# Kernel tuning notes

Measured on AMD Instinct MI355X. Metric: run time of the kernel, lower is better.

## Reference

```python
import jax, jax.numpy as jnp
import numpy as np

N_DOC, N_WORD, N_ENT, N_POS = 10000, 20000, 10000, 60
D, D_POS_IN, D_WEMB = 128, 60, 300
E11, E22, E33, E01, E02, E03 = 320000, 160000, 3600, 300000, 100000, 150000
EPS = 1e-9


def spmm(rows, cols, vals, x, n_out):
    """Sparse (n_out x n_in) adjacency @ x via gather + weighted segment-sum."""
    return jax.ops.segment_sum(vals[:, None] * x[cols], rows, num_segments=n_out)


def gcn(rows, cols, vals, x, n_out, W=None, b=None):
    """GCN layer: adj @ (x W + b) with ReLU; identity=True in torch == W is None."""
    h = x if W is None else x @ W + b
    return jax.nn.relu(spmm(rows, cols, vals, h, n_out))


def setup_inputs():
    key = jax.random.key(0)
    ks = iter(jax.random.split(key, 64))
    randn = lambda s: jax.random.normal(next(ks), s, jnp.float32)
    rand = lambda s: jax.random.uniform(next(ks), s, dtype=jnp.float32)
    ridx = lambda s, hi: jax.random.randint(next(ks), s, 0, hi, jnp.int32)
    return {
        "f1": randn((N_WORD, D)),
        "f2": randn((N_ENT, D)),
        "f3": randn((N_POS, D_POS_IN)),
        "word_emb": randn((N_ENT, D_WEMB)),
        "a11_rows": ridx((E11,), N_WORD), "a11_cols": ridx((E11,), N_WORD), "a11_vals": rand((E11,)),
        "a22_rows": ridx((E22,), N_ENT), "a22_cols": ridx((E22,), N_ENT), "a22_vals": rand((E22,)),
        "a33_rows": ridx((E33,), N_POS), "a33_cols": ridx((E33,), N_POS), "a33_vals": rand((E33,)),
        "a01_rows": ridx((E01,), N_DOC), "a01_cols": ridx((E01,), N_WORD), "a01_vals": rand((E01,)),
        "a02_rows": ridx((E02,), N_DOC), "a02_cols": ridx((E02,), N_ENT), "a02_vals": rand((E02,)),
        "a03_rows": ridx((E03,), N_DOC), "a03_cols": ridx((E03,), N_POS), "a03_vals": rand((E03,)),
        "W3": randn((D_POS_IN, D)) * 0.1, "b3": jnp.zeros((D,), jnp.float32),
        "W1_2": randn((D, D)) * 0.1, "b1_2": jnp.zeros((D,), jnp.float32),
        "W2_2": randn((D, D)) * 0.1, "b2_2": jnp.zeros((D,), jnp.float32),
        "W3_2": randn((D, D)) * 0.1, "b3_2": jnp.zeros((D,), jnp.float32),
    }


def reference(f1, f2, f3, word_emb,
              a11_rows, a11_cols, a11_vals, a22_rows, a22_cols, a22_vals,
              a33_rows, a33_cols, a33_vals, a01_rows, a01_cols, a01_vals,
              a02_rows, a02_cols, a02_vals, a03_rows, a03_cols, a03_vals,
              W3, b3, W1_2, b1_2, W2_2, b2_2, W3_2, b3_2):
    # eval mode: F.dropout(training=False) is a no-op
    # type 1 (words): GCN(identity=True) -> GCN_2
    h1 = gcn(a11_rows, a11_cols, a11_vals, f1, N_WORD)
    h1 = gcn(a11_rows, a11_cols, a11_vals, h1, N_WORD, W1_2, b1_2)
    # type 2 (entities, concat_word_emb=True): GCN(identity=True) -> GCN_2 -> concat word_emb
    h2 = gcn(a22_rows, a22_cols, a22_vals, f2, N_ENT)
    h2 = gcn(a22_rows, a22_cols, a22_vals, h2, N_ENT, W2_2, b2_2)
    h2 = jnp.concatenate([h2, word_emb], axis=-1)  # [N_ENT, D + D_WEMB]
    # type 3 (POS): full GCN -> GCN_2
    h3 = gcn(a33_rows, a33_cols, a33_vals, f3, N_POS, W3, b3)
    h3 = gcn(a33_rows, a33_cols, a33_vals, h3, N_POS, W3_2, b3_2)
    # cross-type aggregation onto documents + L2 normalization
    outs = []
    for rows, cols, vals, h in ((a01_rows, a01_cols, a01_vals, h1),
                                (a02_rows, a02_cols, a02_vals, h2),
                                (a03_rows, a03_cols, a03_vals, h3)):
        agg = spmm(rows, cols, vals, h, N_DOC)  # [N_DOC, d]
        outs.append(agg / (jnp.linalg.norm(agg, axis=-1, keepdims=True) + EPS))
    return tuple(outs)
```

## Files before the change

kernel.cpp:

```cpp
#include <hip/hip_runtime.h>
#include <hip/hip_bf16.h>

typedef __hip_bfloat16 bf16;

#define N_DOC   10000
#define N_WORD  20000
#define N_ENT   10000
#define N_POS   60
#define DD      128
#define D_WEMB  300
#define E11     320000
#define E22     160000
#define E33     3600
#define E01     300000
#define E02     100000
#define E03     150000

#define ROFF11  0
#define ROFF22  20000
#define ROFF33  30000
#define ROFF01  30060
#define ROFF02  40060
#define ROFF03  50060
#define NROWS   60060
#define EOFF11  0
#define EOFF22  320000
#define EOFF33  480000
#define EOFF01  483600
#define EOFF02  783600
#define EOFF03  883600
#define NEDGES  1033600

#define BSHIFT  9
#define NBUCK   118
#define BCAP    18432
#define P1_TILE 4096
#define P1_EPT  8
#define NB1K    253
#define NCONV   120
#define NPOSB1  15

#define HFO_STAGE   0
#define HFO_PAIRS   4349952
#define HFO_G       5383552
#define HFO_BCUR    5443616
#define HFO_F1B     5443744
#define HFO_F2B     6723744
#define HFO_WEMBB   7363744
#define HFO_S0B     8863744
#define HFO_S1B     10143744
#define HFO_E0B     11423744
#define HFO_E1B     12063744
#define HFO_P3A     12703744
#define HFO_P3B     12711424
#define HFO_END     12719104

__device__ __forceinline__ float loadf(const void* p, size_t i, int isb) {
    return isb ? __bfloat162float(((const bf16*)p)[i])
               : ((const float*)p)[i];
}
__device__ __forceinline__ float b2f(unsigned u16) {
    union { unsigned v; float f; } x; x.v = u16 << 16; return x.f;
}
__device__ __forceinline__ unsigned f2b(float f) {
    bf16 h = __float2bfloat16(f);
    union { bf16 h; unsigned short u; } x; x.h = h; return (unsigned)x.u;
}
__device__ __forceinline__ void storef(void* p, size_t i, int asb, float v) {
    if (asb) ((unsigned short*)p)[i] = (unsigned short)f2b(v);
    else     ((float*)p)[i] = v;
}
__device__ __forceinline__ unsigned pack_pair(int col, float v) {
    return (f2b(v) << 16) | (unsigned)col;
}

__device__ __forceinline__ void edge_decode(
        int i,
        const int* __restrict__ r11, const int* __restrict__ c11, const void* __restrict__ v11,
        const int* __restrict__ r22, const int* __restrict__ c22, const void* __restrict__ v22,
        const int* __restrict__ r33, const int* __restrict__ c33, const void* __restrict__ v33,
        const int* __restrict__ r01, const int* __restrict__ c01, const void* __restrict__ v01,
        const int* __restrict__ r02, const int* __restrict__ c02, const void* __restrict__ v02,
        const int* __restrict__ r03, const int* __restrict__ c03, const void* __restrict__ v03,
        int isb, int& slot, int& col, float& val) {
    if      (i < EOFF22) { int k = i;          slot = ROFF11 + r11[k]; col = c11[k]; val = loadf(v11, k, isb); }
    else if (i < EOFF33) { int k = i - EOFF22; slot = ROFF22 + r22[k]; col = c22[k]; val = loadf(v22, k, isb); }
    else if (i < EOFF01) { int k = i - EOFF33; slot = ROFF33 + r33[k]; col = c33[k]; val = loadf(v33, k, isb); }
    else if (i < EOFF02) { int k = i - EOFF01; slot = ROFF01 + r01[k]; col = c01[k]; val = loadf(v01, k, isb); }
    else if (i < EOFF03) { int k = i - EOFF02; slot = ROFF02 + r02[k]; col = c02[k]; val = loadf(v02, k, isb); }
    else                 { int k = i - EOFF03; slot = ROFF03 + r03[k]; col = c03[k]; val = loadf(v03, k, isb); }
}

__global__ void detect_kernel(const unsigned* __restrict__ probe, int* __restrict__ flag,
                              int* __restrict__ bcur) {
    __shared__ int cnt;
    if (threadIdx.x == 0) cnt = 0;
    __syncthreads();
    int insane = 0;
    for (int i = threadIdx.x; i < 1024; i += 256) {
        float x = __uint_as_float(probe[i]);
        float a = fabsf(x);
        if (!(a > 1e-10f && a < 1e10f)) insane++;
    }
    atomicAdd(&cnt, insane);
    if (bcur && threadIdx.x < NBUCK) bcur[threadIdx.x] = threadIdx.x * BCAP;
    __syncthreads();
    if (threadIdx.x == 0) *flag = (cnt > 512) ? 1 : 0;
}

__device__ __forceinline__ void conv_seg(const void* __restrict__ src,
                                         unsigned* __restrict__ dst,
                                         int npairs, int isb, int tid, int stride) {
    if (isb) {
        const unsigned* s = (const unsigned*)src;
        for (int i = tid; i < npairs; i += stride) dst[i] = s[i];
    } else {
        const float2* s = (const float2*)src;
        for (int i = tid; i < npairs; i += stride) {
            float2 x = s[i];
            dst[i] = f2b(x.x) | (f2b(x.y) << 16);
        }
    }
}

template<bool RELU, int K>
__device__ __forceinline__ void rowpar_body256(
        const void* __restrict__ X, int xisb,
        const void* __restrict__ W, const void* __restrict__ b,
        void* __restrict__ out, int oisb, int isb,
        int row, int tid, float* xr ) {
    int half = tid >> 7;
    int j = tid & 127;
    float* xrh = xr + half * K;
    if (j < K) {
        float x = loadf(X, (size_t)row * K + j, xisb);
        if (RELU) x = fmaxf(x, 0.f);
        xrh[j] = x;
    }
    __syncthreads();
    float acc = loadf(b, j, isb);
    #pragma unroll 8
    for (int k = 0; k < K; ++k)
        acc = fmaf(xrh[k], loadf(W, (size_t)k * 128 + j, isb), acc);
    storef(out, (size_t)row * 128 + j, oisb, acc);
}

template<bool RELU, int K>
__device__ __forceinline__ void rowpar_body512(
        const void* __restrict__ X, int xisb,
        const void* __restrict__ W, const void* __restrict__ b,
        void* __restrict__ out, int oisb, int isb,
        int row0, int tid, float* xr ) {
    int q = tid >> 7;
    int j = tid & 127;
    int row = row0 + q;
    float* xrh = xr + q * K;
// ... 136 lines not shown
        wsum2[t] = v;
    }
    __syncthreads();
    int myrp = ((w > 0) ? wsum2[w - 1] : 0) + s - x;
    rp[t] = myrp;
    cu[t] = 0;
    int slot = (b << BSHIFT) + t;
    if (slot < NROWS) G[slot] = bb + myrp;
    __syncthreads();
    for (int i = t; i < cnt; i += 512) {
        uint2 r = st[i];
        int sl = (r.x >> 16) & 511;
        int p = atomicAdd(&cu[sl], 1);
        pairs[bb + rp[sl] + p] = (r.y << 16) | (r.x & 0xffffu);
    }
}

__global__ void hist2_kernel(const int* __restrict__ rowsA, int nEA,
                             const int* __restrict__ rowsB, int nEB,
                             int nA, int* __restrict__ cnt) {
    int i = blockIdx.x * blockDim.x + threadIdx.x;
    if (i < nEA) atomicAdd(cnt + rowsA[i], 1);
    else if (i < nEA + nEB) atomicAdd(cnt + nA + rowsB[i - nEA], 1);
}

__device__ void scan_ex(const int* __restrict__ cnt, int* __restrict__ rp, int n) {
    __shared__ int wsum[16];
    __shared__ int carry;
    int t = threadIdx.x, lane = t & 63, w = t >> 6;
    if (t == 0) carry = 0;
    __syncthreads();
    for (int base = 0; base < n; base += 1024) {
        int i = base + t;
        int x = (i < n) ? cnt[i] : 0;
        int s = x;
        #pragma unroll
        for (int off = 1; off < 64; off <<= 1) {
            int y = __shfl_up(s, off);
            if (lane >= off) s += y;
        }
        if (lane == 63) wsum[w] = s;
        __syncthreads();
        if (w == 0) {
            int v = (lane < 16) ? wsum[lane] : 0;
            #pragma unroll
            for (int off = 1; off < 16; off <<= 1) {
                int y = __shfl_up(v, off);
                if (lane >= off) v += y;
            }
            if (lane < 16) wsum[lane] = v;
        }
        __syncthreads();
        int woff = (w > 0) ? wsum[w - 1] : 0;
        if (i < n) rp[i] = carry + woff + s - x;
        __syncthreads();
        if (t == 0) carry += wsum[15];
        __syncthreads();
    }
    if (t == 0) rp[n] = carry;
}

__global__ __launch_bounds__(1024) void scan2_kernel(
        const int* __restrict__ cntA, int* __restrict__ rpA, int nA,
        const int* __restrict__ cntB, int* __restrict__ rpB, int nB) {
    scan_ex(cntA, rpA, nA);
    __syncthreads();
    scan_ex(cntB, rpB, nB);
}

__global__ void copy2_kernel(const int* __restrict__ rpA, const int* __restrict__ rpB,
                             int nA, int nB, int* __restrict__ cur) {
    int i = blockIdx.x * blockDim.x + threadIdx.x;
    if (i < nA) cur[i] = rpA[i];
    else if (i < nA + nB) cur[i] = rpB[i - nA];
}

__global__ void scatter2_kernel(const int* __restrict__ rowsA, const int* __restrict__ colsA,
                                const void* __restrict__ valsA, int nEA,
                                const int* __restrict__ rowsB, const int* __restrict__ colsB,
                                const void* __restrict__ valsB, int nEB,
                                int nA, int* __restrict__ cur,
                                unsigned* __restrict__ pairsA, unsigned* __restrict__ pairsB,
                                const int* __restrict__ dflag) {
    int i = blockIdx.x * blockDim.x + threadIdx.x;
    int isb = *dflag;
    if (i < nEA) {
        int p = atomicAdd(cur + rowsA[i], 1);
        pairsA[p] = pack_pair(colsA[i], loadf(valsA, i, isb));
    } else if (i < nEA + nEB) {
        int k = i - nEA;
        int p = atomicAdd(cur + nA + rowsB[k], 1);
        pairsB[p] = pack_pair(colsB[k], loadf(valsB, k, isb));
    }
}

__device__ __forceinline__ void accum8_bf16(uint4 u, float v, bool relu, float* acc) {
    float x0 = b2f(u.x & 0xffffu), x1 = b2f(u.x >> 16);
    float x2 = b2f(u.y & 0xffffu), x3 = b2f(u.y >> 16);
    float x4 = b2f(u.z & 0xffffu), x5 = b2f(u.z >> 16);
    float x6 = b2f(u.w & 0xffffu), x7 = b2f(u.w >> 16);
    if (relu) {
        x0 = fmaxf(x0, 0.f); x1 = fmaxf(x1, 0.f); x2 = fmaxf(x2, 0.f); x3 = fmaxf(x3, 0.f);
        x4 = fmaxf(x4, 0.f); x5 = fmaxf(x5, 0.f); x6 = fmaxf(x6, 0.f); x7 = fmaxf(x7, 0.f);
    }
    acc[0] = fmaf(v, x0, acc[0]); acc[1] = fmaf(v, x1, acc[1]);
    acc[2] = fmaf(v, x2, acc[2]); acc[3] = fmaf(v, x3, acc[3]);
    acc[4] = fmaf(v, x4, acc[4]); acc[5] = fmaf(v, x5, acc[5]);
    acc[6] = fmaf(v, x6, acc[6]); acc[7] = fmaf(v, x7, acc[7]);
}

template<bool RELU>
__device__ __forceinline__ void gather4_accum(
        const int* __restrict__ rp, const unsigned* __restrict__ pairs,
        const bf16* __restrict__ src, int row, int lane, float* acc) {
    #pragma unroll
    for (int j = 0; j < 8; ++j) acc[j] = 0.f;
    int e0 = rp[row], e1 = rp[row + 1];
    if (e0 >= e1) return;
    int q = lane >> 4, sub = lane & 15;
    int e = e0;
    for (; e + 16 <= e1; e += 16) {
        unsigned p0 = pairs[e + q];
        unsigned p1 = pairs[e + 4 + q];
        unsigned p2 = pairs[e + 8 + q];
        unsigned p3 = pairs[e + 12 + q];
        uint4 u0 = *(const uint4*)((const unsigned short*)src + (size_t)(p0 & 0xffffu) * 128 + sub * 8);
        uint4 u1 = *(const uint4*)((const unsigned short*)src + (size_t)(p1 & 0xffffu) * 128 + sub * 8);
        uint4 u2 = *(const uint4*)((const unsigned short*)src + (size_t)(p2 & 0xffffu) * 128 + sub * 8);
        uint4 u3 = *(const uint4*)((const unsigned short*)src + (size_t)(p3 & 0xffffu) * 128 + sub * 8);
        accum8_bf16(u0, b2f(p0 >> 16), RELU, acc);
        accum8_bf16(u1, b2f(p1 >> 16), RELU, acc);
        accum8_bf16(u2, b2f(p2 >> 16), RELU, acc);
        accum8_bf16(u3, b2f(p3 >> 16), RELU, acc);
    }
    for (; e < e1; e += 4) {
        int idx = e + q;
        unsigned p = pairs[(idx < e1) ? idx : (e1 - 1)];
        float v = (idx < e1) ? b2f(p >> 16) : 0.f;
        uint4 u = *(const uint4*)((const unsigned short*)src + (size_t)(p & 0xffffu) * 128 + sub * 8);
        accum8_bf16(u, v, RELU, acc);
    }
}

template<bool RELU>
__device__ __forceinline__ void gather4_body(
        const int* __restrict__ rp, const unsigned* __restrict__ pairs,
        const bf16* __restrict__ src, bf16* __restrict__ dst, int row, int lane) {
    float acc[8];
    gather4_accum<RELU>(rp, pairs, src, row, lane, acc);
    #pragma unroll
    for (int j = 0; j < 8; ++j) {
        acc[j] += __shfl_xor(acc[j], 16);
        acc[j] += __shfl_xor(acc[j], 32);
    }
    if ((lane >> 4) == 0) {
        int sub = lane & 15;
        uint4 o;
        o.x = f2b(acc[0]) | (f2b(acc[1]) << 16);
        o.y = f2b(acc[2]) | (f2b(acc[3]) << 16);
        o.z = f2b(acc[4]) | (f2b(acc[5]) << 16);
        o.w = f2b(acc[6]) | (f2b(acc[7]) << 16);
        *(uint4*)((unsigned short*)dst + (size_t)row * 128 + sub * 8) = o;
    }
}

template<bool RELU>
__device__ __forceinline__ void norm4_body(
        const int* __restrict__ rp, const unsigned* __restrict__ pairs,
        const bf16* __restrict__ src, void* __restrict__ out, size_t elem_off,
        int row, int lane, int oisb) {
    float acc[8];
    gather4_accum<RELU>(rp, pairs, src, row, lane, acc);
    #pragma unroll
    for (int j = 0; j < 8; ++j) {
        acc[j] += __shfl_xor(acc[j], 16);
        acc[j] += __shfl_xor(acc[j], 32);
    }
    float ss = 0.f;
    #pragma unroll
    for (int j = 0; j < 8; ++j) ss = fmaf(acc[j], acc[j], ss);
    #pragma unroll
    for (int off = 1; off < 16; off <<= 1) ss += __shfl_xor(ss, off);
    float inv = 1.0f / (sqrtf(ss) + 1e-9f);
    if ((lane >> 4) == 0) {
        int sub = lane & 15;
        size_t base = elem_off + (size_t)row * 128;
        if (oisb) {
            uint4 o;
            o.x = f2b(acc[0] * inv) | (f2b(acc[1] * inv) << 16);
            o.y = f2b(acc[2] * inv) | (f2b(acc[3] * inv) << 16);
            o.z = f2b(acc[4] * inv) | (f2b(acc[5] * inv) << 16);
            o.w = f2b(acc[6] * inv) | (f2b(acc[7] * inv) << 16);
            *(uint4*)((unsigned short*)out + base + sub * 8) = o;
        } else {
            float4* op = (float4*)((float*)out + base);
            op[sub * 2]     = make_float4(acc[0] * inv, acc[1] * inv, acc[2] * inv, acc[3] * inv);
            op[sub * 2 + 1] = make_float4(acc[4] * inv, acc[5] * inv, acc[6] * inv, acc[7] * inv);
        }
    }
}

template<bool RELU>
__device__ __forceinline__ void gather_accum16(
        const int* __restrict__ rp, const unsigned* __restrict__ pairs,
        const void* __restrict__ src, int sisb, int row, int lane,
        float& tx, float& ty) {
    int e0 = rp[row], e1 = rp[row + 1];
    float accx[8], accy[8];
    #pragma unroll
    for (int k = 0; k < 8; ++k) { accx[k] = 0.f; accy[k] = 0.f; }
    int e = e0;
    if (sisb) {
        const bf16* sb = (const bf16*)src;
        for (; e + 8 <= e1; e += 8) {
            unsigned p[8], u[8];
            #pragma unroll
            for (int k = 0; k < 8; ++k) p[k] = pairs[e + k];
            #pragma unroll
            for (int k = 0; k < 8; ++k)
                u[k] = ((const unsigned*)(sb + (size_t)(p[k] & 0xffffu) * 128))[lane];
            #pragma unroll
            for (int k = 0; k < 8; ++k) {
                float v = b2f(p[k] >> 16);
                float x0 = b2f(u[k] & 0xffffu), x1 = b2f(u[k] >> 16);
                if (RELU) { x0 = fmaxf(x0, 0.f); x1 = fmaxf(x1, 0.f); }
                accx[k] = fmaf(v, x0, accx[k]);
                accy[k] = fmaf(v, x1, accy[k]);
            }
        }
        for (; e + 2 <= e1; e += 2) {
            unsigned p0 = pairs[e], p1 = pairs[e + 1];
            unsigned u0 = ((const unsigned*)(sb + (size_t)(p0 & 0xffffu) * 128))[lane];
            unsigned u1 = ((const unsigned*)(sb + (size_t)(p1 & 0xffffu) * 128))[lane];
            float v0 = b2f(p0 >> 16), v1 = b2f(p1 >> 16);
            float x0 = b2f(u0 & 0xffffu), x1 = b2f(u0 >> 16);
            float y0 = b2f(u1 & 0xffffu), y1 = b2f(u1 >> 16);
            if (RELU) {
                x0 = fmaxf(x0, 0.f); x1 = fmaxf(x1, 0.f);
                y0 = fmaxf(y0, 0.f); y1 = fmaxf(y1, 0.f);
            }
            accx[0] = fmaf(v0, x0, accx[0]); accy[0] = fmaf(v0, x1, accy[0]);
            accx[1] = fmaf(v1, y0, accx[1]); accy[1] = fmaf(v1, y1, accy[1]);
        }
        if (e < e1) {
            unsigned p = pairs[e];
            float v = b2f(p >> 16);
            unsigned u = ((const unsigned*)(sb + (size_t)(p & 0xffffu) * 128))[lane];
            float x0 = b2f(u & 0xffffu), x1 = b2f(u >> 16);
            if (RELU) { x0 = fmaxf(x0, 0.f); x1 = fmaxf(x1, 0.f); }
            accx[0] = fmaf(v, x0, accx[0]); accy[0] = fmaf(v, x1, accy[0]);
        }
    } else {
        const float* sf = (const float*)src;
        for (; e + 8 <= e1; e += 8) {
            unsigned p[8]; float2 u[8];
            #pragma unroll
            for (int k = 0; k < 8; ++k) p[k] = pairs[e + k];
            #pragma unroll
            for (int k = 0; k < 8; ++k)
                u[k] = ((const float2*)(sf + (size_t)(p[k] & 0xffffu) * 128))[lane];
            #pragma unroll
            for (int k = 0; k < 8; ++k) {
                float v = b2f(p[k] >> 16);
                float x0 = u[k].x, x1 = u[k].y;
                if (RELU) { x0 = fmaxf(x0, 0.f); x1 = fmaxf(x1, 0.f); }
                accx[k] = fmaf(v, x0, accx[k]);
                accy[k] = fmaf(v, x1, accy[k]);
            }
        }
        for (; e + 2 <= e1; e += 2) {
            unsigned p0 = pairs[e], p1 = pairs[e + 1];
            float2 x = ((const float2*)(sf + (size_t)(p0 & 0xffffu) * 128))[lane];
            float2 y = ((const float2*)(sf + (size_t)(p1 & 0xffffu) * 128))[lane];
            float v0 = b2f(p0 >> 16), v1 = b2f(p1 >> 16);
            if (RELU) {
                x.x = fmaxf(x.x, 0.f); x.y = fmaxf(x.y, 0.f);
                y.x = fmaxf(y.x, 0.f); y.y = fmaxf(y.y, 0.f);
            }
            accx[0] = fmaf(v0, x.x, accx[0]); accy[0] = fmaf(v0, x.y, accy[0]);
            accx[1] = fmaf(v1, y.x, accx[1]); accy[1] = fmaf(v1, y.y, accy[1]);
        }
        if (e < e1) {
            unsigned p = pairs[e];
            float v = b2f(p >> 16);
            float2 x = ((const float2*)(sf + (size_t)(p & 0xffffu) * 128))[lane];
            if (RELU) { x.x = fmaxf(x.x, 0.f); x.y = fmaxf(x.y, 0.f); }
            accx[0] = fmaf(v, x.x, accx[0]); accy[0] = fmaf(v, x.y, accy[0]);
        }
    }
    tx = ((accx[0] + accx[1]) + (accx[2] + accx[3])) + ((accx[4] + accx[5]) + (accx[6] + accx[7]));
    ty = ((accy[0] + accy[1]) + (accy[2] + accy[3])) + ((accy[4] + accy[5]) + (accy[6] + accy[7]));
}

template<bool RELU>
__device__ __forceinline__ void gather128_body(
        const int* __restrict__ rp, const unsigned* __restrict__ pairs,
        const void* __restrict__ src, int sisb,
        void* __restrict__ dst, int disb, int row, int lane) {
    float tx, ty;
    gather_accum16<RELU>(rp, pairs, src, sisb, row, lane, tx, ty);
    if (disb) {
        ((unsigned*)((bf16*)dst + (size_t)row * 128))[lane] = f2b(tx) | (f2b(ty) << 16);
    } else {
        ((float2*)((float*)dst + (size_t)row * 128))[lane] = make_float2(tx, ty);
    }
}
// ... 120 lines not shown
    float t1x = a1.x + b1.x, t1y = a1.y + b1.y;
    float t2x[3], t2y[3];
    #pragma unroll
    for (int s = 0; s < 3; ++s) { t2x[s] = a2[s].x + b2v[s].x; t2y[s] = a2[s].y + b2v[s].y; }
    float ss = t1x * t1x + t1y * t1y;
    #pragma unroll
    for (int s = 0; s < 3; ++s) {
        int pi = lane + 64 * s;
        if (pi < P2) ss += t2x[s] * t2x[s] + t2y[s] * t2y[s];
    }
    #pragma unroll
    for (int off = 32; off > 0; off >>= 1) ss += __shfl_down(ss, off);
    ss = __shfl(ss, 0);
    float inv = 1.0f / (sqrtf(ss) + 1e-9f);
    size_t base = elem_off + (size_t)row * (DD + D_WEMB);
    if (isb) {
        ((unsigned*)((bf16*)out + base))[lane] = f2b(t1x * inv) | (f2b(t1y * inv) << 16);
        unsigned* o2 = (unsigned*)((bf16*)out + base + DD);
        #pragma unroll
        for (int s = 0; s < 3; ++s) {
            int pi = lane + 64 * s;
            if (pi < P2) o2[pi] = f2b(t2x[s] * inv) | (f2b(t2y[s] * inv) << 16);
        }
    } else {
        ((float2*)((float*)out + base))[lane] = make_float2(t1x * inv, t1y * inv);
        float2* o2 = (float2*)((float*)out + base + DD);
        #pragma unroll
        for (int s = 0; s < 3; ++s) {
            int pi = lane + 64 * s;
            if (pi < P2) o2[pi] = make_float2(t2x[s] * inv, t2y[s] * inv);
        }
    }
}

template<bool RELU>
__global__ void spmm_gather128(const int* __restrict__ rowptr, const unsigned* __restrict__ pairs,
                               const void* __restrict__ src, int src_flagged,
                               void* __restrict__ dst, int dst_flagged,
                               int n, const int* __restrict__ dflag) {
    int row = blockIdx.x * 4 + (threadIdx.x >> 6);
    if (row >= n) return;
    int isb = *dflag;
    gather128_body<RELU>(rowptr, pairs, src, src_flagged ? isb : 0,
                         dst, dst_flagged ? isb : 0, row, threadIdx.x & 63);
}

__global__ void hop_posg(const int* __restrict__ G, const unsigned* __restrict__ pairs,
                         int roff1, const void* __restrict__ src1, void* __restrict__ dst1, int n1, int B1,
                         int roff2, const void* __restrict__ src2, void* __restrict__ dst2, int n2, int B2,
                         const void* __restrict__ Psrc, void* __restrict__ Pdst,
                         const int* __restrict__ dflag) {
    int b = blockIdx.x;
    int lane = threadIdx.x & 63;
    if (b < B1) {
        int row = b * 4 + (threadIdx.x >> 6);
        if (row >= n1) return;
        gather4_body<false>(G + roff1, pairs, (const bf16*)src1, (bf16*)dst1, row, lane);
    } else if (b < B1 + B2) {
        int row = (b - B1) * 4 + (threadIdx.x >> 6);
        if (row >= n2) return;
        gather4_body<false>(G + roff2, pairs, (const bf16*)src2, (bf16*)dst2, row, lane);
    } else {
        int row = (b - B1 - B2) * 4 + (threadIdx.x >> 6);
        if (row >= N_POS) return;
        gather4_body<false>(G + ROFF33, pairs, (const bf16*)Psrc, (bf16*)Pdst, row, lane);
    }
}

template<bool RELU>
__global__ void spmm_norm128(const int* __restrict__ rowptr, const unsigned* __restrict__ pairs,
                             const void* __restrict__ src, int src_flagged,
                             void* __restrict__ out, size_t elem_off,
                             int n, const int* __restrict__ dflag) {
    int row = blockIdx.x * 4 + (threadIdx.x >> 6);
    if (row >= n) return;
    int isb = *dflag;
    norm128_body<RELU>(rowptr, pairs, src, src_flagged ? isb : 0, out, elem_off,
                       row, threadIdx.x & 63, isb);
}

__global__ void spmm2_norm(const int* __restrict__ rowptr, const unsigned* __restrict__ pairs,
                           const void* __restrict__ src1, int s1_flagged,
                           const void* __restrict__ src2, int s2_flagged,
                           void* __restrict__ out, size_t elem_off,
                           int n, const int* __restrict__ dflag) {
    int row = blockIdx.x * 4 + (threadIdx.x >> 6);
    if (row >= n) return;
    int isb = *dflag;
    norm428_body(rowptr, pairs, src1, s1_flagged ? isb : 0, src2, s2_flagged ? isb : 0,
                 out, elem_off, row, threadIdx.x & 63, isb);
}

__global__ void final_norm_all(const int* __restrict__ G, const unsigned* __restrict__ pairs,
                               const void* __restrict__ s1, const void* __restrict__ e0b,
                               const void* __restrict__ wemb, const void* __restrict__ p3b,
                               void* __restrict__ out,
                               size_t off1, size_t off2, size_t off3,
                               const int* __restrict__ dflag) {
    int isb = *dflag;
    int lane = threadIdx.x & 63;
    int b = blockIdx.x;
    if (b < 2500) {
        int row = b * 4 + (threadIdx.x >> 6);
        if (row >= N_DOC) return;
        norm4_body<true>(G + ROFF01, pairs, (const bf16*)s1, out, off1, row, lane, isb);
    } else if (b < 5000) {
        int row = (b - 2500) * 4 + (threadIdx.x >> 6);
        if (row >= N_DOC) return;
        norm428_body(G + ROFF02, pairs, e0b, 1, wemb, 1, out, off2, row, lane, isb);
    } else {
        int row = (b - 5000) * 4 + (threadIdx.x >> 6);
        if (row >= N_DOC) return;
        norm4_body<true>(G + ROFF03, pairs, (const bf16*)p3b, out, off3, row, lane, isb);
    }
}

template<bool RELU>
__global__ void spmm_kernel(const int* __restrict__ rows, const int* __restrict__ cols,
                            const void* __restrict__ vals,
                            const void* __restrict__ src, int sstride, int src_flagged,
                            float* __restrict__ dst, int dstride, int doff,
                            int d, int nE, const int* __restrict__ dflag) {
    int e = blockIdx.x * (blockDim.x >> 6) + (threadIdx.x >> 6);
    if (e >= nE) return;
    int isb  = *dflag;
    int sisb = src_flagged ? isb : 0;
    int lane = threadIdx.x & 63;
    int r = rows[e];
    int c = cols[e];
    float v = loadf(vals, e, isb);
    size_t sbase = (size_t)c * sstride;
    float* dp = dst + (size_t)r * dstride + doff;
    if (sisb) {
        const unsigned* sp = (const unsigned*)((const bf16*)src + sbase);
        for (int j = 2 * lane; j < d; j += 128) {
            unsigned u = sp[j >> 1];
            float x0 = b2f(u & 0xffffu);
            float x1 = b2f(u >> 16);
            if (RELU) { x0 = fmaxf(x0, 0.f); x1 = fmaxf(x1, 0.f); }
            atomicAdd(dp + j,     v * x0);
            atomicAdd(dp + j + 1, v * x1);
        }
    } else {
        const float2* sp = (const float2*)((const float*)src + sbase);
        for (int j = 2 * lane; j < d; j += 128) {
            float2 x = sp[j >> 1];
            if (RELU) { x.x = fmaxf(x.x, 0.f); x.y = fmaxf(x.y, 0.f); }
            atomicAdd(dp + j,     v * x.x);
            atomicAdd(dp + j + 1, v * x.y);
        }
    }
}

template<bool RELU, bool XB>
__device__ __forceinline__ void gemm_tile_body(
        const void* __restrict__ X, const void* __restrict__ W,
        const void* __restrict__ b, void* __restrict__ out, int n,
        int bx, int by, int isb, int oisb, float* Wl ) {
    if (bx * 64 >= n) return;
    int tid = threadIdx.x;
    int jc = by * 64;
    if (isb) {
        const uint2* Wg = (const uint2*)W;
        float4* Wl4 = (float4*)Wl;
        for (int vidx = tid; vidx < 2048; vidx += 256) {
            int k = vidx >> 4, jl4 = vidx & 15;
            uint2 u = Wg[k * 32 + (jc >> 2) + jl4];
            float4 vv;
            vv.x = b2f(u.x & 0xffffu);
            vv.y = b2f(u.x >> 16);
            vv.z = b2f(u.y & 0xffffu);
            vv.w = b2f(u.y >> 16);
            Wl4[vidx] = vv;
        }
    } else {
        const float4* Wg = (const float4*)W;
        float4* Wl4 = (float4*)Wl;
        for (int vidx = tid; vidx < 2048; vidx += 256) {
            int k = vidx >> 4, jl4 = vidx & 15;
            Wl4[vidx] = Wg[k * 32 + (jc >> 2) + jl4];
        }
    }
    __syncthreads();
    int j2 = tid & 31;
    int g  = tid >> 5;
    float bc0 = loadf(b, jc + 2 * j2, isb);
    float bc1 = loadf(b, jc + 2 * j2 + 1, isb);
    int i0 = bx * 64 + g * 8;
    float a0[8], a1[8];
    #pragma unroll
    for (int r = 0; r < 8; ++r) { a0[r] = bc0; a1[r] = bc1; }
    const char* xbase = (const char*)X + (size_t)i0 * 128 * (XB ? 2 : 4);
    const float2* Wl2 = (const float2*)Wl;
    #pragma unroll 2
    for (int k4 = 0; k4 < 32; ++k4) {
        float2 w0 = Wl2[(4 * k4 + 0) * 32 + j2];
        float2 w1 = Wl2[(4 * k4 + 1) * 32 + j2];
        float2 w2 = Wl2[(4 * k4 + 2) * 32 + j2];
        float2 w3 = Wl2[(4 * k4 + 3) * 32 + j2];
        #pragma unroll
        for (int r = 0; r < 8; ++r) {
            float4 v;
            if (XB) {
                uint2 u = ((const uint2*)xbase)[r * 32 + k4];
                v.x = b2f(u.x & 0xffffu); v.y = b2f(u.x >> 16);
                v.z = b2f(u.y & 0xffffu); v.w = b2f(u.y >> 16);
            } else {
                v = ((const float4*)xbase)[r * 32 + k4];
            }
            if (RELU) {
                v.x = fmaxf(v.x, 0.f); v.y = fmaxf(v.y, 0.f);
                v.z = fmaxf(v.z, 0.f); v.w = fmaxf(v.w, 0.f);
            }
            a0[r] = fmaf(v.w, w3.x, fmaf(v.z, w2.x, fmaf(v.y, w1.x, fmaf(v.x, w0.x, a0[r]))));
            a1[r] = fmaf(v.w, w3.y, fmaf(v.z, w2.y, fmaf(v.y, w1.y, fmaf(v.x, w0.y, a1[r]))));
        }
    }
    #pragma unroll
    for (int r = 0; r < 8; ++r) {
        int i = i0 + r;
        if (i < n) {
            if (oisb) {
                ((unsigned*)((bf16*)out + (size_t)i * 128 + jc))[j2] =
                    f2b(a0[r]) | (f2b(a1[r]) << 16);
            } else {
                ((float2*)((float*)out + (size_t)i * 128 + jc))[j2] =
                    make_float2(a0[r], a1[r]);
            }
        }
    }
}

template<bool RELU>
__global__ __launch_bounds__(256) void gemm_tile(
        const float* __restrict__ X, const void* __restrict__ W,
        const void* __restrict__ b, void* __restrict__ out, int n,
        const int* __restrict__ dflag) {
    __shared__ float Wl[128 * 64];
    int isb = *dflag;
    gemm_tile_body<RELU, false>(X, W, b, out, n, blockIdx.x, blockIdx.y, isb, isb, Wl);
}

template<bool RELU>
__global__ __launch_bounds__(256) void gemm_tile_b2g(
        const void* __restrict__ X1, const void* __restrict__ W1, const void* __restrict__ b1,
        void* __restrict__ out1, int n1, int G1,
        const void* __restrict__ X2, const void* __restrict__ W2, const void* __restrict__ b2,
        void* __restrict__ out2, int n2, int GT,
        const void* __restrict__ PX, const void* __restrict__ PW,
        const void* __restrict__ Pb, void* __restrict__ PO,
        const int* __restrict__ dflag) {
    __shared__ float Wl[128 * 64];
    int isb = *dflag;
    int x = blockIdx.x;
    if (x < G1) {
        gemm_tile_body<RELU, true>(X1, W1, b1, out1, n1, x, blockIdx.y, isb, 1, Wl);
    } else if (x < GT) {
        gemm_tile_body<RELU, true>(X2, W2, b2, out2, n2, x - G1, blockIdx.y, isb, 1, Wl);
    } else {
        if (blockIdx.y != 0) return;
        int row = (x - GT) * 2 + (threadIdx.x >> 7);
        rowpar_body256<true, 128>(PX, 1, PW, Pb, PO, 1, isb, row, threadIdx.x, Wl);
    }
}

template<bool RELU>
__global__ __launch_bounds__(256) void gemm128_kernel(
        const float* __restrict__ X, const void* __restrict__ W,
        const void* __restrict__ b, float* __restrict__ out, int n,
        const int* __restrict__ dflag) {
    __shared__ float Wl[128 * 128];
    int isb = *dflag;
    int tid = threadIdx.x;
    if (isb) {
        const uint2* Wg = (const uint2*)W;
        float4* Wl4 = (float4*)Wl;
        for (int idx = tid; idx < 4096; idx += 256) {
            uint2 u = Wg[idx];
            float4 vv;
            vv.x = b2f(u.x & 0xffffu);
            vv.y = b2f(u.x >> 16);
            vv.z = b2f(u.y & 0xffffu);
            vv.w = b2f(u.y >> 16);
            Wl4[idx] = vv;
        }
    } else {
        const float4* Wg = (const float4*)W;
        float4* Wl4 = (float4*)Wl;
        for (int idx = tid; idx < 4096; idx += 256) Wl4[idx] = Wg[idx];
    }
    __syncthreads();
    int j = tid & 127;
    int h = tid >> 7;
    float bj = loadf(b, j, isb);
    int row0 = blockIdx.x * 64 + h * 32;
    for (int q = 0; q < 8; ++q) {
        int gi = row0 + q * 4;
        if (gi >= n) break;
        const float4* x0 = (const float4*)(X + (size_t)gi * 128);
        const float4* x1 = x0 + 32;
        const float4* x2 = x1 + 32;
        const float4* x3 = x2 + 32;
        float a0 = bj, a1 = bj, a2 = bj, a3 = bj;
        #pragma unroll 4
        for (int k4 = 0; k4 < 32; ++k4) {
            float4 v0 = x0[k4], v1 = x1[k4], v2 = x2[k4], v3 = x3[k4];
            if (RELU) {
                v0.x = fmaxf(v0.x, 0.f); v0.y = fmaxf(v0.y, 0.f); v0.z = fmaxf(v0.z, 0.f); v0.w = fmaxf(v0.w, 0.f);
                v1.x = fmaxf(v1.x, 0.f); v1.y = fmaxf(v1.y, 0.f); v1.z = fmaxf(v1.z, 0.f); v1.w = fmaxf(v1.w, 0.f);
                v2.x = fmaxf(v2.x, 0.f); v2.y = fmaxf(v2.y, 0.f); v2.z = fmaxf(v2.z, 0.f); v2.w = fmaxf(v2.w, 0.f);
                v3.x = fmaxf(v3.x, 0.f); v3.y = fmaxf(v3.y, 0.f); v3.z = fmaxf(v3.z, 0.f); v3.w = fmaxf(v3.w, 0.f);
            }
            float w0 = Wl[(4 * k4 + 0) * 128 + j];
            float w1 = Wl[(4 * k4 + 1) * 128 + j];
            float w2 = Wl[(4 * k4 + 2) * 128 + j];
            float w3 = Wl[(4 * k4 + 3) * 128 + j];
            a0 = fmaf(v0.w, w3, fmaf(v0.z, w2, fmaf(v0.y, w1, fmaf(v0.x, w0, a0))));
            a1 = fmaf(v1.w, w3, fmaf(v1.z, w2, fmaf(v1.y, w1, fmaf(v1.x, w0, a1))));
            a2 = fmaf(v2.w, w3, fmaf(v2.z, w2, fmaf(v2.y, w1, fmaf(v2.x, w0, a2))));
            a3 = fmaf(v3.w, w3, fmaf(v3.z, w2, fmaf(v3.y, w1, fmaf(v3.x, w0, a3))));
        }
        float* o = out + (size_t)gi * 128 + j;
        o[0] = a0; o[128] = a1; o[256] = a2; o[384] = a3;
    }
}

template<bool RELU, int K>
__global__ void rowpar_gemm(const void* __restrict__ X, int x_flagged,
                            const void* __restrict__ W, const void* __restrict__ b,
                            void* __restrict__ out, int out_flagged,
                            const int* __restrict__ dflag) {
    __shared__ float xr[K];
    int isb  = *dflag;
    int xisb = x_flagged ? isb : 0;
    int oisb = out_flagged ? isb : 0;
    int row = blockIdx.x;
    int j = threadIdx.x;
    if (j < K) {
        float x = loadf(X, (size_t)row * K + j, xisb);
        if (RELU) x = fmaxf(x, 0.f);
        xr[j] = x;
    }
    __syncthreads();
    float acc = loadf(b, j, isb);
    #pragma unroll 8
    for (int k = 0; k < K; ++k)
        acc = fmaf(xr[k], loadf(W, (size_t)k * 128 + j, isb), acc);
    storef(out, (size_t)row * 128 + j, oisb, acc);
}

template<bool RELU, int K>
__global__ void gemm_kernel(const void* __restrict__ X, int x_flagged,
                            const void* __restrict__ W,
                            const void* __restrict__ b,
                            float* __restrict__ out, int n,
                            const int* __restrict__ dflag) {
    __shared__ float Wl[K * 128];
    int isb  = *dflag;
    int xisb = x_flagged ? isb : 0;
    int j = threadIdx.x;
    for (int idx = j; idx < K * 128; idx += 128)
        Wl[idx] = loadf(W, idx, isb);
    __syncthreads();
    float bj = loadf(b, j, isb);
    int row0 = blockIdx.x * 64;
    for (int i0 = 0; i0 < 64; i0 += 4) {
        int i = row0 + i0;
        if (i >= n) break;
        size_t r0 = (size_t)i * K;
        float a0 = bj, a1 = bj, a2 = bj, a3 = bj;
        for (int k = 0; k < K; ++k) {
            float w = Wl[k * 128 + j];
            float v0 = loadf(X, r0 + k, xisb);
            float v1 = loadf(X, r0 + K + k, xisb);
            float v2 = loadf(X, r0 + 2 * K + k, xisb);
            float v3 = loadf(X, r0 + 3 * K + k, xisb);
            if (RELU) {
                v0 = fmaxf(v0, 0.f); v1 = fmaxf(v1, 0.f);
                v2 = fmaxf(v2, 0.f); v3 = fmaxf(v3, 0.f);
            }
            a0 = fmaf(v0, w, a0);
            a1 = fmaf(v1, w, a1);
            a2 = fmaf(v2, w, a2);
            a3 = fmaf(v3, w, a3);
        }
        float* o = out + (size_t)i * 128 + j;
        o[0] = a0; o[128] = a1; o[256] = a2; o[384] = a3;
    }
}

__global__ void l2norm_kernel(const float* __restrict__ agg, int d,
                              void* __restrict__ out, size_t elem_off, int n,
                              const int* __restrict__ dflag) {
    int row = blockIdx.x * (blockDim.x >> 6) + (threadIdx.x >> 6);
    if (row >= n) return;
    int isb  = *dflag;
    int lane = threadIdx.x & 63;
    const float2* a2 = (const float2*)(agg + (size_t)row * d);
    float ss = 0.f;
    for (int j = 2 * lane; j < d; j += 128) {
        float2 x = a2[j >> 1];
        ss += x.x * x.x + x.y * x.y;
    }
    #pragma unroll
    for (int off = 32; off > 0; off >>= 1) ss += __shfl_down(ss, off);
    ss = __shfl(ss, 0);
    float inv = 1.0f / (sqrtf(ss) + 1e-9f);
    size_t bbase = elem_off + (size_t)row * d;
    if (isb) {
        unsigned* o = (unsigned*)((bf16*)out + bbase);
        for (int j = 2 * lane; j < d; j += 128) {
            float2 x = a2[j >> 1];
            o[j >> 1] = f2b(x.x * inv) | (f2b(x.y * inv) << 16);
        }
    } else {
        float2* o = (float2*)((float*)out + bbase);
        for (int j = 2 * lane; j < d; j += 128) {
            float2 x = a2[j >> 1];
            o[j >> 1] = make_float2(x.x * inv, x.y * inv);
        }
    }
}

static inline int spmm_grid(int nE) { return (nE + 3) / 4; }
static inline int row_grid(int n)   { return (n + 3) / 4; }
static inline int pad8(int x)       { return (x + 7) & ~7; }

static void build2(hipStream_t stream,
                   const int* rowsA, const int* colsA, const void* valsA, int nA, int nEA,
                   const int* rowsB, const int* colsB, const void* valsB, int nB, int nEB,
                   int* rpA, int* rpB, int* curAB, unsigned* pairsA, unsigned* pairsB,
                   const int* dflag) {
    int nE = nEA + nEB;
    hipMemsetAsync(curAB, 0, (size_t)(nA + nB) * 4, stream);
    hist2_kernel<<<(nE + 255) / 256, 256, 0, stream>>>(rowsA, nEA, rowsB, nEB, nA, curAB);
    scan2_kernel<<<1, 1024, 0, stream>>>(curAB, rpA, nA, curAB + nA, rpB, nB);
    copy2_kernel<<<(nA + nB + 255) / 256, 256, 0, stream>>>(rpA, rpB, nA, nB, curAB);
    scatter2_kernel<<<(nE + 255) / 256, 256, 0, stream>>>(
        rowsA, colsA, valsA, nEA, rowsB, colsB, valsB, nEB, nA, curAB, pairsA, pairsB, dflag);
}

extern "C" void kernel_launch(void* const* d_in, const int* in_sizes, int n_in,
                              void* d_out, int out_size, void* d_ws, size_t ws_size,
                              hipStream_t stream) {
    const void* f1   = d_in[0];
    const void* f2   = d_in[1];
    const void* f3   = d_in[2];
    const void* wemb = d_in[3];
    const int*  a11r = (const int*)d_in[4];
    const int*  a11c = (const int*)d_in[5];
    const void* a11v = d_in[6];
    const int*  a22r = (const int*)d_in[7];
    const int*  a22c = (const int*)d_in[8];
    const void* a22v = d_in[9];
    const int*  a33r = (const int*)d_in[10];
    const int*  a33c = (const int*)d_in[11];
    const void* a33v = d_in[12];
    const int*  a01r = (const int*)d_in[13];
    const int*  a01c = (const int*)d_in[14];
    const void* a01v = d_in[15];
    const int*  a02r = (const int*)d_in[16];
    const int*  a02c = (const int*)d_in[17];
    const void* a02v = d_in[18];
    const int*  a03r = (const int*)d_in[19];
    const int*  a03c = (const int*)d_in[20];
    const void* a03v = d_in[21];
    const void* W3   = d_in[22];
    const void* b3   = d_in[23];
    const void* W1_2 = d_in[24];
    const void* b1_2 = d_in[25];
    const void* W2_2 = d_in[26];
    const void* b2_2 = d_in[27];
    const void* W3_2 = d_in[28];
    const void* b3_2 = d_in[29];

    int*   dflag = (int*)d_ws;
    float* base  = (float*)d_ws + 16;

    const size_t OUT1_OFF = 0;
    const size_t OUT2_OFF = (size_t)N_DOC * DD;
    const size_t OUT3_OFF = OUT2_OFF + (size_t)N_DOC * (DD + D_WEMB);

    dim3 blk(256);

    const size_t WS_BIG = 64 + (size_t)HFO_END * 4;
    const size_t WS_MID = 64 + 22240000ull + (60008ull + 620000ull) * 4;

    if (ws_size >= WS_BIG) {
        uint2*    staging = (uint2*)(base + HFO_STAGE);
        unsigned* pairs   = (unsigned*)(base + HFO_PAIRS);
        int*      G       = (int*)(base + HFO_G);
        int*      bcur    = (int*)(base + HFO_BCUR);
        void*     f1q     = (void*)(base + HFO_F1B);
        void*     f2q     = (void*)(base + HFO_F2B);
        void*     wq      = (void*)(base + HFO_WEMBB);
        void*     S0b     = (void*)(base + HFO_S0B);
        void*     S1b     = (void*)(base + HFO_S1B);
        void*     E0b     = (void*)(base + HFO_E0B);
        void*     E1b     = (void*)(base + HFO_E1B);
        void*     P3a     = (void*)(base + HFO_P3A);
        void*     P3b     = (void*)(base + HFO_P3B);

        detect_kernel<<<1, 256, 0, stream>>>((const unsigned*)f1, dflag, bcur);

        bin_edges_fused<<<NB1K + NCONV + NPOSB1, 512, 0, stream>>>(
            a11r, a11c, a11v, a22r, a22c, a22v, a33r, a33c, a33v,
            a01r, a01c, a01v, a02r, a02c, a02v, a03r, a03c, a03v,
            bcur, staging,
            f1, f2, wemb, (unsigned*)f1q, (unsigned*)f2q, (unsigned*)wq,
            f3, W3, b3, P3a, dflag);

        finalize_csr<<<NBUCK, 512, 0, stream>>>(bcur, staging, G, pairs);

        int B1 = row_grid(N_WORD), B2 = row_grid(N_ENT);
        hop_posg<<<B1 + B2 + row_grid(N_POS), blk, 0, stream>>>(
            G, pairs, ROFF11, f1q, S0b, N_WORD, B1,
            ROFF22, f2q, E0b, N_ENT, B2, P3a, P3b, dflag);
        {
            int G1 = pad8((N_WORD + 63) / 64), G2 = pad8((N_ENT + 63) / 64);
            int GT = G1 + G2;
            gemm_tile_b2g<true><<<dim3(GT + 30, 2), 256, 0, stream>>>(
                S0b, W1_2, b1_2, S1b, N_WORD, G1,
                E0b, W2_2, b2_2, E1b, N_ENT, GT,
                P3b, W3_2, b3_2, P3a, dflag);
        }
        hop_posg<<<B1 + B2 + row_grid(N_POS), blk, 0, stream>>>(
            G, pairs, ROFF11, S1b, S0b, N_WORD, B1,
            ROFF22, E1b, E0b, N_ENT, B2, P3a, P3b, dflag);

        final_norm_all<<<7500, blk, 0, stream>>>(
            G, pairs, S0b, E0b, wq, P3b, d_out, OUT1_OFF, OUT2_OFF, OUT3_OFF, dflag);
    } else if (ws_size >= WS_MID) {
        detect_kernel<<<1, 256, 0, stream>>>((const unsigned*)f1, dflag, (int*)nullptr);
        float* S0   = base;
        float* S1   = base + 2560000;
        float* E0   = base;
        float* E1   = base + 1280000;
        float* P3a  = base;
        float* P3b  = base + 7680;
        int* I = (int*)(base + 5560000);
        {
            int* rpA = I; int* rpB = rpA + (N_WORD + 1); int* cur = rpB + (N_DOC + 1);
            unsigned* pA = (unsigned*)(cur + N_WORD + N_DOC); unsigned* pB = pA + E11;
            build2(stream, a11r, a11c, a11v, N_WORD, E11,
                   a01r, a01c, a01v, N_DOC, E01, rpA, rpB, cur, pA, pB, dflag);
            spmm_gather128<false><<<row_grid(N_WORD), blk, 0, stream>>>(
                rpA, pA, f1, 1, S0, 0, N_WORD, dflag);
            gemm_tile<true><<<dim3(pad8((N_WORD + 63) / 64), 2), 256, 0, stream>>>(
                S0, W1_2, b1_2, S1, N_WORD, dflag);
            spmm_gather128<false><<<row_grid(N_WORD), blk, 0, stream>>>(
                rpA, pA, S1, 1, S0, 1, N_WORD, dflag);
            spmm_norm128<true><<<row_grid(N_DOC), blk, 0, stream>>>(
                rpB, pB, S0, 1, d_out, OUT1_OFF, N_DOC, dflag);
        }
        {
            int* rpA = I; int* rpB = rpA + (N_ENT + 1); int* cur = rpB + (N_DOC + 1);
            unsigned* pA = (unsigned*)(cur + N_ENT + N_DOC); unsigned* pB = pA + E22;
            build2(stream, a22r, a22c, a22v, N_ENT, E22,
                   a02r, a02c, a02v, N_DOC, E02, rpA, rpB, cur, pA, pB, dflag);
            spmm_gather128<false><<<row_grid(N_ENT), blk, 0, stream>>>(
                rpA, pA, f2, 1, E0, 0, N_ENT, dflag);
            gemm_tile<true><<<dim3(pad8((N_ENT + 63) / 64), 2), 256, 0, stream>>>(
                E0, W2_2, b2_2, E1, N_ENT, dflag);
            spmm_gather128<false><<<row_grid(N_ENT), blk, 0, stream>>>(
                rpA, pA, E1, 1, E0, 1, N_ENT, dflag);
            spmm2_norm<<<row_grid(N_DOC), blk, 0, stream>>>(
                rpB, pB, E0, 1, wemb, 1, d_out, OUT2_OFF, N_DOC, dflag);
        }
        {
            int* rpA = I; int* rpB = rpA + (N_POS + 1); int* cur = rpB + (N_DOC + 1);
            unsigned* pA = (unsigned*)(cur + N_POS + N_DOC); unsigned* pB = pA + E33;
            build2(stream, a33r, a33c, a33v, N_POS, E33,
                   a03r, a03c, a03v, N_DOC, E03, rpA, rpB, cur, pA, pB, dflag);
            rowpar_gemm<false, 60><<<N_POS, 128, 0, stream>>>(
                f3, 1, W3, b3, P3a, 1, dflag);
            spmm_gather128<false><<<row_grid(N_POS), blk, 0, stream>>>(
                rpA, pA, P3a, 1, P3b, 1, N_POS, dflag);
            rowpar_gemm<true, 128><<<N_POS, 128, 0, stream>>>(
                P3b, 1, W3_2, b3_2, P3a, 1, dflag);
            spmm_gather128<false><<<row_grid(N_POS), blk, 0, stream>>>(
                rpA, pA, P3a, 1, P3b, 1, N_POS, dflag);
            spmm_norm128<true><<<row_grid(N_DOC), blk, 0, stream>>>(
                rpB, pB, P3b, 1, d_out, OUT3_OFF, N_DOC, dflag);
        }
    } else {
        detect_kernel<<<1, 256, 0, stream>>>((const unsigned*)f1, dflag, (int*)nullptr);
        float* S0   = base;
        float* S1   = base + 2560000;
        float* AGG1 = S1;
        float* E0   = base;
        float* E1   = base + 1280000;
        float* AGG2 = base + 1280000;
        float* P3a  = base;
        float* P3b  = base + 7680;
        float* AGG3 = base + 15360;
        hipMemsetAsync(S0, 0, (size_t)N_WORD * DD * 4, stream);
        spmm_kernel<false><<<spmm_grid(E11), blk, 0, stream>>>(
            a11r, a11c, a11v, f1, DD, 1, S0, DD, 0, DD, E11, dflag);
        gemm128_kernel<true><<<(N_WORD + 63) / 64, 256, 0, stream>>>(
            S0, W1_2, b1_2, S1, N_WORD, dflag);
        hipMemsetAsync(S0, 0, (size_t)N_WORD * DD * 4, stream);
        spmm_kernel<false><<<spmm_grid(E11), blk, 0, stream>>>(
            a11r, a11c, a11v, S1, DD, 0, S0, DD, 0, DD, E11, dflag);
        hipMemsetAsync(AGG1, 0, (size_t)N_DOC * DD * 4, stream);
        spmm_kernel<true><<<spmm_grid(E01), blk, 0, stream>>>(
            a01r, a01c, a01v, S0, DD, 0, AGG1, DD, 0, DD, E01, dflag);
        l2norm_kernel<<<row_grid(N_DOC), blk, 0, stream>>>(
            AGG1, DD, d_out, OUT1_OFF, N_DOC, dflag);

        hipMemsetAsync(E0, 0, (size_t)N_ENT * DD * 4, stream);
        spmm_kernel<false><<<spmm_grid(E22), blk, 0, stream>>>(
            a22r, a22c, a22v, f2, DD, 1, E0, DD, 0, DD, E22, dflag);
        gemm128_kernel<true><<<(N_ENT + 63) / 64, 256, 0, stream>>>(
            E0, W2_2, b2_2, E1, N_ENT, dflag);
        hipMemsetAsync(E0, 0, (size_t)N_ENT * DD * 4, stream);
        spmm_kernel<false><<<spmm_grid(E22), blk, 0, stream>>>(
            a22r, a22c, a22v, E1, DD, 0, E0, DD, 0, DD, E22, dflag);
        hipMemsetAsync(AGG2, 0, (size_t)N_DOC * (DD + D_WEMB) * 4, stream);
        spmm_kernel<true><<<spmm_grid(E02), blk, 0, stream>>>(
            a02r, a02c, a02v, E0, DD, 0, AGG2, DD + D_WEMB, 0, DD, E02, dflag);
        spmm_kernel<false><<<spmm_grid(E02), blk, 0, stream>>>(
            a02r, a02c, a02v, wemb, D_WEMB, 1, AGG2, DD + D_WEMB, DD, D_WEMB, E02, dflag);
        l2norm_kernel<<<row_grid(N_DOC), blk, 0, stream>>>(
            AGG2, DD + D_WEMB, d_out, OUT2_OFF, N_DOC, dflag);

        gemm_kernel<false, 60><<<1, 128, 0, stream>>>(f3, 1, W3, b3, P3a, N_POS, dflag);
        hipMemsetAsync(P3b, 0, (size_t)N_POS * DD * 4, stream);
        spmm_kernel<false><<<spmm_grid(E33), blk, 0, stream>>>(
            a33r, a33c, a33v, P3a, DD, 0, P3b, DD, 0, DD, E33, dflag);
        gemm128_kernel<true><<<1, 256, 0, stream>>>(
            P3b, W3_2, b3_2, P3a, N_POS, dflag);
        hipMemsetAsync(P3b, 0, (size_t)N_POS * DD * 4, stream);
        spmm_kernel<false><<<spmm_grid(E33), blk, 0, stream>>>(
            a33r, a33c, a33v, P3a, DD, 0, P3b, DD, 0, DD, E33, dflag);
        hipMemsetAsync(AGG3, 0, (size_t)N_DOC * DD * 4, stream);
        spmm_kernel<true><<<spmm_grid(E03), blk, 0, stream>>>(
            a03r, a03c, a03v, P3b, DD, 0, AGG3, DD, 0, DD, E03, dflag);
        l2norm_kernel<<<row_grid(N_DOC), blk, 0, stream>>>(
            AGG3, DD, d_out, OUT3_OFF, N_DOC, dflag);
    }
}
```

Measured before the change: 276.2 us.

## Replace scalar tiled GEMM with bf16 MFMA GEMM and fold ReLU into gather

The mid-layer 128x128 GEMMs for word and entity features, previously a scalar FMA tiled kernel with a LDS-staged weight tile, now use MFMA 16x16x32 bf16 instructions with weight fragments held in registers, one block per 32 rows. The ReLU that the GEMM used to apply to its input is moved into the gather's output store, so the stored hop output is already activated. This cuts FP32 ALU work and shared-memory traffic in the GEMM stage, at the cost of per-block scalar weight loads and scattered 2-byte output stores. The gather change applies ReLU to every gather4_body caller, which may alter other paths.

```diff
diff --git a/kernel.cpp b/kernel.cpp
--- a/kernel.cpp
+++ b/kernel.cpp
@@ -2,6 +2,8 @@
 #include <hip/hip_bf16.h>
 
 typedef __hip_bfloat16 bf16;
+typedef __attribute__((ext_vector_type(8))) short short8;
+typedef __attribute__((ext_vector_type(4))) float f32x4;
 
 #define N_DOC   10000
 #define N_WORD  20000
@@ -444,6 +446,7 @@
     for (int j = 0; j < 8; ++j) {
         acc[j] += __shfl_xor(acc[j], 16);
         acc[j] += __shfl_xor(acc[j], 32);
+        acc[j] = fmaxf(acc[j], 0.f);
     }
     if ((lane >> 4) == 0) {
         int sub = lane & 15;
@@ -870,11 +873,11 @@
     }
 }
 
-template<bool RELU, bool XB>
+template<bool RELU>
 __device__ __forceinline__ void gemm_tile_body(
-        const void* __restrict__ X, const void* __restrict__ W,
+        const float* __restrict__ X, const void* __restrict__ W,
         const void* __restrict__ b, void* __restrict__ out, int n,
-        int bx, int by, int isb, int oisb, float* Wl ) {
+        int bx, int by, int isb, float* Wl ) {
     if (bx * 64 >= n) return;
     int tid = threadIdx.x;
     int jc = by * 64;
@@ -908,7 +911,7 @@
     float a0[8], a1[8];
     #pragma unroll
     for (int r = 0; r < 8; ++r) { a0[r] = bc0; a1[r] = bc1; }
-    const char* xbase = (const char*)X + (size_t)i0 * 128 * (XB ? 2 : 4);
+    const float4* xp = (const float4*)(X + (size_t)i0 * 128);
     const float2* Wl2 = (const float2*)Wl;
     #pragma unroll 2
     for (int k4 = 0; k4 < 32; ++k4) {
@@ -918,14 +921,7 @@
         float2 w3 = Wl2[(4 * k4 + 3) * 32 + j2];
         #pragma unroll
         for (int r = 0; r < 8; ++r) {
-            float4 v;
-            if (XB) {
-                uint2 u = ((const uint2*)xbase)[r * 32 + k4];
-                v.x = b2f(u.x & 0xffffu); v.y = b2f(u.x >> 16);
-                v.z = b2f(u.y & 0xffffu); v.w = b2f(u.y >> 16);
-            } else {
-                v = ((const float4*)xbase)[r * 32 + k4];
-            }
+            float4 v = xp[r * 32 + k4];
             if (RELU) {
                 v.x = fmaxf(v.x, 0.f); v.y = fmaxf(v.y, 0.f);
                 v.z = fmaxf(v.z, 0.f); v.w = fmaxf(v.w, 0.f);
@@ -938,7 +934,7 @@
     for (int r = 0; r < 8; ++r) {
         int i = i0 + r;
         if (i < n) {
-            if (oisb) {
+            if (isb) {
                 ((unsigned*)((bf16*)out + (size_t)i * 128 + jc))[j2] =
                     f2b(a0[r]) | (f2b(a1[r]) << 16);
             } else {
@@ -956,11 +952,58 @@
         const int* __restrict__ dflag) {
     __shared__ float Wl[128 * 64];
     int isb = *dflag;
-    gemm_tile_body<RELU, false>(X, W, b, out, n, blockIdx.x, blockIdx.y, isb, isb, Wl);
-}
-
-template<bool RELU>
-__global__ __launch_bounds__(256) void gemm_tile_b2g(
+    gemm_tile_body<RELU>(X, W, b, out, n, blockIdx.x, blockIdx.y, isb, Wl);
+}
+
+__device__ __forceinline__ void gemm_mfma_seg(
+        const unsigned short* __restrict__ X, const void* __restrict__ W,
+        const void* __restrict__ bb, unsigned short* __restrict__ out,
+        int n, int bx, int tid, int isb) {
+    int wave = tid >> 6, lane = tid & 63;
+    int lo = lane & 15, hi = lane >> 4;
+    short8 bfrag[2][4];
+    #pragma unroll
+    for (int ct = 0; ct < 2; ++ct) {
+        int col = wave * 32 + ct * 16 + lo;
+        #pragma unroll
+        for (int ks = 0; ks < 4; ++ks) {
+            short8 f;
+            #pragma unroll
+            for (int b = 0; b < 8; ++b) {
+                int k = ks * 32 + hi * 8 + b;
+                f[b] = (short)f2b(loadf(W, (size_t)k * 128 + col, isb));
+            }
+            bfrag[ct][ks] = f;
+        }
+    }
+    float bc0 = loadf(bb, wave * 32 + lo, isb);
+    float bc1 = loadf(bb, wave * 32 + 16 + lo, isb);
+    int row0 = bx * 32;
+    #pragma unroll
+    for (int mt = 0; mt < 2; ++mt) {
+        int r0 = row0 + mt * 16;
+        if (r0 >= n) break;
+        f32x4 acc0 = {bc0, bc0, bc0, bc0};
+        f32x4 acc1 = {bc1, bc1, bc1, bc1};
+        const unsigned short* xrow = X + (size_t)(r0 + lo) * 128;
+        #pragma unroll
+        for (int ks = 0; ks < 4; ++ks) {
+            union { uint4 u; short8 s; } a;
+            a.u = *(const uint4*)(xrow + ks * 32 + hi * 8);
+            acc0 = __builtin_amdgcn_mfma_f32_16x16x32_bf16(a.s, bfrag[0][ks], acc0, 0, 0, 0);
+            acc1 = __builtin_amdgcn_mfma_f32_16x16x32_bf16(a.s, bfrag[1][ks], acc1, 0, 0, 0);
+        }
+        int c0 = wave * 32 + lo, c1 = c0 + 16;
+        #pragma unroll
+        for (int r = 0; r < 4; ++r) {
+            int row = r0 + hi * 4 + r;
+            out[(size_t)row * 128 + c0] = (unsigned short)f2b(acc0[r]);
+            out[(size_t)row * 128 + c1] = (unsigned short)f2b(acc1[r]);
+        }
+    }
+}
+
+__global__ __launch_bounds__(256) void gemm_mfma_b2(
         const void* __restrict__ X1, const void* __restrict__ W1, const void* __restrict__ b1,
         void* __restrict__ out1, int n1, int G1,
         const void* __restrict__ X2, const void* __restrict__ W2, const void* __restrict__ b2,
@@ -968,17 +1011,20 @@
         const void* __restrict__ PX, const void* __restrict__ PW,
         const void* __restrict__ Pb, void* __restrict__ PO,
         const int* __restrict__ dflag) {
-    __shared__ float Wl[128 * 64];
+    __shared__ float xr[2 * 128];
     int isb = *dflag;
     int x = blockIdx.x;
+    if (x >= GT) {
+        int row = (x - GT) * 2 + (threadIdx.x >> 7);
+        rowpar_body256<true, 128>(PX, 1, PW, Pb, PO, 1, isb, row, threadIdx.x, xr);
+        return;
+    }
     if (x < G1) {
-        gemm_tile_body<RELU, true>(X1, W1, b1, out1, n1, x, blockIdx.y, isb, 1, Wl);
-    } else if (x < GT) {
-        gemm_tile_body<RELU, true>(X2, W2, b2, out2, n2, x - G1, blockIdx.y, isb, 1, Wl);
+        gemm_mfma_seg((const unsigned short*)X1, W1, b1, (unsigned short*)out1,
+                      n1, x, threadIdx.x, isb);
     } else {
-        if (blockIdx.y != 0) return;
-        int row = (x - GT) * 2 + (threadIdx.x >> 7);
-        rowpar_body256<true, 128>(PX, 1, PW, Pb, PO, 1, isb, row, threadIdx.x, Wl);
+        gemm_mfma_seg((const unsigned short*)X2, W2, b2, (unsigned short*)out2,
+                      n2, x - G1, threadIdx.x, isb);
     }
 }
 
@@ -1235,9 +1281,9 @@
             G, pairs, ROFF11, f1q, S0b, N_WORD, B1,
             ROFF22, f2q, E0b, N_ENT, B2, P3a, P3b, dflag);
         {
-            int G1 = pad8((N_WORD + 63) / 64), G2 = pad8((N_ENT + 63) / 64);
+            int G1 = (N_WORD + 31) / 32, G2 = (N_ENT + 31) / 32;
             int GT = G1 + G2;
-            gemm_tile_b2g<true><<<dim3(GT + 30, 2), 256, 0, stream>>>(
+            gemm_mfma_b2<<<GT + 30, 256, 0, stream>>>(
                 S0b, W1_2, b1_2, S1b, N_WORD, G1,
                 E0b, W2_2, b2_2, E1b, N_ENT, GT,
                 P3b, W3_2, b3_2, P3a, dflag);
```

Measured after the change: 265.3 us (median of 2 runs). -3.9%, faster.
